# Kernel tuning notes

Measured on AMD Instinct MI355X. Metric: run time of the kernel, lower is better.

Reference implementation:

```python
import jax, jax.numpy as jnp
import numpy as np

N_NODES = 100000
N_EDGES = 640000
N_GRAPHS = 2048
HID = 128
L = 3


def setup_inputs() -> dict:
    key = jax.random.key(0)
    ks = jax.random.split(key, 24)
    f32 = jnp.float32
    x = jax.random.normal(ks[0], (N_NODES, 7), dtype=f32)
    edge_attr = jax.random.normal(ks[1], (N_EDGES, 3), dtype=f32)
    edge_index = jax.random.randint(ks[2], (2, N_EDGES), 0, N_NODES, dtype=jnp.int32)
    batch = jnp.sort(jax.random.randint(ks[3], (N_NODES,), 0, N_GRAPHS, dtype=jnp.int32))

    def lin(k, fi, fo):
        return jax.random.normal(k, (fi, fo), dtype=f32) / jnp.sqrt(jnp.asarray(fi, f32))

    inp = dict(x=x, edge_attr=edge_attr, edge_index=edge_index, batch=batch)
    inp["node_w"] = lin(ks[4], 7, HID); inp["node_b"] = jnp.zeros((HID,), f32)
    inp["ew1"] = lin(ks[5], 3, HID);   inp["eb1"] = jnp.zeros((HID,), f32)
    inp["ew2"] = lin(ks[6], HID, HID); inp["eb2"] = jnp.zeros((HID,), f32)
    inp["cw1"] = jnp.stack([lin(ks[7 + i], HID, HID) for i in range(L)])
    inp["cb1"] = jnp.zeros((L, HID), f32)
    inp["cw2"] = jnp.stack([lin(ks[10 + i], HID, HID) for i in range(L)])
    inp["cb2"] = jnp.zeros((L, HID), f32)
    inp["clw1"] = lin(ks[13], HID, 64); inp["clb1"] = jnp.zeros((64,), f32)
    inp["clw2"] = lin(ks[14], 64, 1);   inp["clb2"] = jnp.zeros((1,), f32)
    inp["rw1"] = lin(ks[15], HID, 64);  inp["rb1"] = jnp.zeros((64,), f32)
    inp["rw2"] = lin(ks[16], 64, 1);    inp["rb2"] = jnp.zeros((1,), f32)
    return inp


def reference(x, edge_attr, node_w, node_b, ew1, eb1, ew2, eb2,
              cw1, cb1, cw2, cb2, clw1, clb1, clw2, clb2,
              rw1, rb1, rw2, rb2, edge_index, batch):
    relu = jax.nn.relu
    # encoders
    h = x @ node_w + node_b                                   # [N, H]
    e = relu(edge_attr @ ew1 + eb1) @ ew2 + eb2               # [E, H]
    src, dst = edge_index[0], edge_index[1]
    for l in range(L):
        # GINEConv (eps=0): out = MLP(h_i + sum_j ReLU(h_j + e_ji))
        m = relu(h[src] + e)                                  # [E, H] gather + edge add
        agg = jax.ops.segment_sum(m, dst, num_segments=N_NODES)
        z = h + agg
        h = relu(z @ cw1[l] + cb1[l]) @ cw2[l] + cb2[l]
        h = relu(h)                                           # dropout = identity (eval)
    # global mean pool
    ones = jnp.ones((h.shape[0],), h.dtype)
    counts = jax.ops.segment_sum(ones, batch, num_segments=N_GRAPHS)
    g = jax.ops.segment_sum(h, batch, num_segments=N_GRAPHS) / jnp.maximum(counts, 1.0)[:, None]
    success_logit = (relu(g @ clw1 + clb1) @ clw2 + clb2)[:, 0]
    route_length = (relu(g @ rw1 + rb1) @ rw2 + rb2)[:, 0]
    return success_logit, route_length
```

## Files before the change

### kernel.cpp

```cpp
#include <hip/hip_runtime.h>

#define HID 128
#define LDP 136

typedef short s16x8 __attribute__((ext_vector_type(8)));
typedef float f32x4 __attribute__((ext_vector_type(4)));
typedef float f32x2 __attribute__((ext_vector_type(2)));

__device__ __forceinline__ float bf2f(unsigned int u) {
  union { unsigned int i; float f; } v; v.i = u << 16; return v.f;
}
__device__ __forceinline__ float asf(unsigned int u) {
  union { unsigned int i; float f; } v; v.i = u; return v.f;
}
__device__ __forceinline__ unsigned short f2bf(float f) {
  union { float f; unsigned int i; } v; v.f = f;
  unsigned int r = v.i + 0x7fffu + ((v.i >> 16) & 1u);
  return (unsigned short)(r >> 16);
}
__device__ __forceinline__ unsigned char f2fp8(float f) {
  unsigned int p = __builtin_amdgcn_cvt_pk_fp8_f32(f, f, 0u, false);
  return (unsigned char)(p & 0xffu);
}

__global__ void k_zero4(float4* __restrict__ p, size_t n4) {
  size_t i = (size_t)blockIdx.x * blockDim.x + threadIdx.x;
  if (i < n4) p[i] = (float4){0.f, 0.f, 0.f, 0.f};
}

__global__ void k_hist(const int* __restrict__ dst, int* __restrict__ deg, int nE) {
  int e = blockIdx.x * blockDim.x + threadIdx.x;
  if (e < nE) atomicAdd(&deg[dst[e]], 1);
}

__global__ void k_scanA(const int* __restrict__ deg, int* __restrict__ bsum) {
  __shared__ int ss[256];
  int t = threadIdx.x;
  ss[t] = deg[blockIdx.x * 256 + t];
  __syncthreads();
  for (int off = 128; off; off >>= 1) {
    if (t < off) ss[t] += ss[t + off];
    __syncthreads();
  }
  if (t == 0) bsum[blockIdx.x] = ss[0];
}

__global__ void k_scanB(const int* __restrict__ bsum, int* __restrict__ bsumx, int NB) {
  __shared__ int sd[512];
  int t = threadIdx.x;
  int v = (t < NB) ? bsum[t] : 0;
  sd[t] = v;
  __syncthreads();
  for (int off = 1; off < 512; off <<= 1) {
    int a = (t >= off) ? sd[t - off] : 0;
    __syncthreads();
    sd[t] += a;
    __syncthreads();
  }
  if (t < NB) bsumx[t] = sd[t] - v;
}

__global__ void k_scanC(const int* __restrict__ deg, const int* __restrict__ bsumx,
                        int* __restrict__ cursor, int* __restrict__ rowptr) {
  __shared__ int ss[256];
  int t = threadIdx.x, i = blockIdx.x * 256 + t;
  int v = deg[i];
  ss[t] = v;
  __syncthreads();
  for (int off = 1; off < 256; off <<= 1) {
    int a = (t >= off) ? ss[t - off] : 0;
    __syncthreads();
    ss[t] += a;
    __syncthreads();
  }
  int ex = ss[t] - v + bsumx[blockIdx.x];
  cursor[i] = ex;
  rowptr[i] = ex;
}

__global__ void k_scatter(const int* __restrict__ src, const int* __restrict__ dst,
                          int* __restrict__ cursor,
                          int* __restrict__ src_s, int* __restrict__ esort, int nE) {
  int e = blockIdx.x * blockDim.x + threadIdx.x;
  if (e >= nE) return;
  int d = dst[e];
  int pos = atomicAdd(&cursor[d], 1);
  src_s[pos] = src[e];
  esort[pos] = e;
}

__global__ void k_prep_w(const float* __restrict__ ew2, const float* __restrict__ cw1,
                         const float* __restrict__ cw2, unsigned short* __restrict__ wT) {
  int idx = blockIdx.x * blockDim.x + threadIdx.x;
  if (idx >= 7 * 16384) return;
  int m = idx >> 14, i = idx & 16383;
  int n = i >> 7, k = i & 127;
  const float* s = (m == 0) ? ew2 : (m <= 3 ? cw1 + (size_t)(m - 1) * 16384
                                            : cw2 + (size_t)(m - 4) * 16384);
  wT[idx] = f2bf(s[k * 128 + n]);
}

__global__ void k_node_enc(const float* __restrict__ x, const float* __restrict__ w,
                           const float* __restrict__ b, unsigned short* __restrict__ h16, int nN) {
  int idx = blockIdx.x * blockDim.x + threadIdx.x;
  if (idx >= nN * HID) return;
  int i = idx >> 7, j = idx & 127;
  float acc = b[j];
  const float* xr = x + (size_t)i * 7;
#pragma unroll
  for (int k = 0; k < 7; ++k) acc += xr[k] * w[k * HID + j];
  h16[idx] = f2bf(acc);
}

__global__ void __launch_bounds__(256) k_edge_gemm(
    const float* __restrict__ ea, const int* __restrict__ esort,
    const float* __restrict__ ew1, const float* __restrict__ eb1,
    const unsigned short* __restrict__ w2t, const float* __restrict__ eb2,
    unsigned char* __restrict__ e8, int nE) {
  __shared__ __attribute__((aligned(16))) unsigned short ts1[128 * LDP];
  __shared__ float eaL[384];
  __shared__ int esL[128];
  int tid = threadIdx.x;
  int e0 = blockIdx.x * 128;
  if (tid < 128) esL[tid] = esort[e0 + tid];
  __syncthreads();
  for (int i = tid; i < 384; i += 256) {
    int r = i / 3, c = i - r * 3;
    eaL[i] = ea[(size_t)esL[r] * 3 + c];
  }
  __syncthreads();
  {
    int j = tid & 127, r0 = (tid >> 7) * 64;
    float wa = ew1[j], wb = ew1[HID + j], wc = ew1[2 * HID + j], bj = eb1[j];
    for (int r = r0; r < r0 + 64; ++r) {
      float a = bj + eaL[r * 3] * wa + eaL[r * 3 + 1] * wb + eaL[r * 3 + 2] * wc;
      ts1[r * LDP + j] = f2bf(fmaxf(a, 0.f));
    }
  }
  __syncthreads();
  int wave = tid >> 6, lane = tid & 63;
  int l15 = lane & 15, quad = lane >> 4;
  int rbase = (wave >> 1) * 64, nbase = (wave & 1) * 64;
  f32x4 acc[4][4];
#pragma unroll
  for (int i = 0; i < 4; ++i)
#pragma unroll
    for (int j = 0; j < 4; ++j) acc[i][j] = (f32x4){0.f, 0.f, 0.f, 0.f};
  for (int kc = 0; kc < 4; ++kc) {
    int k0 = kc * 32 + quad * 8;
    s16x8 af[4], bf[4];
#pragma unroll
    for (int t = 0; t < 4; ++t)
      af[t] = *(const s16x8*)&ts1[(rbase + t * 16 + l15) * LDP + k0];
#pragma unroll
    for (int t = 0; t < 4; ++t)
      bf[t] = *(const s16x8*)&w2t[(size_t)(nbase + t * 16 + l15) * HID + k0];
#pragma unroll
    for (int i = 0; i < 4; ++i)
#pragma unroll
      for (int j = 0; j < 4; ++j)
        acc[i][j] = __builtin_amdgcn_mfma_f32_16x16x32_bf16(af[i], bf[j], acc[i][j], 0, 0, 0);
  }
  float ebv[4];
#pragma unroll
  for (int t = 0; t < 4; ++t) ebv[t] = eb2[nbase + t * 16 + l15];
#pragma unroll
  for (int tr = 0; tr < 4; ++tr)
#pragma unroll
    for (int reg = 0; reg < 4; ++reg) {
      int row = rbase + tr * 16 + quad * 4 + reg;
#pragma unroll
      for (int tc = 0; tc < 4; ++tc) {
        int col = nbase + tc * 16 + l15;
        e8[(size_t)(e0 + row) * HID + col] = f2fp8(acc[tr][tc][reg] + ebv[tc]);
      }
    }
}

__global__ void __launch_bounds__(256) k_conv_csr(
    const unsigned short* __restrict__ h16in, const unsigned char* __restrict__ e8,
    const int* __restrict__ src_s, const int* __restrict__ rowptr,
    const unsigned short* __restrict__ w1t, const float* __restrict__ b1,
    const unsigned short* __restrict__ w2t, const float* __restrict__ b2,
    unsigned short* __restrict__ h16out, int nN) {
  __shared__ __attribute__((aligned(16))) unsigned short zs[32 * LDP];
  __shared__ int rpS[4][12];
  int tid = threadIdx.x;
  int n0 = blockIdx.x * 32;
  int wave = tid >> 6, lane = tid & 63;
  int l15 = lane & 15, quad = lane >> 4;
  {
    int c16 = l15 * 8;
    int c2 = lane * 2;
    int wbase = wave * 8;
    int nodeBase = n0 + wbase;
    int nCnt = nN - nodeBase; if (nCnt > 8) nCnt = 8; if (nCnt < 0) nCnt = 0;
#pragma unroll
    for (int i = 0; i < 8; ++i) {
      int n = nodeBase + i;
      unsigned int hv = 0u;
      if (n < nN) hv = *(const unsigned int*)&h16in[(size_t)n * HID + c2];
      *(unsigned int*)&zs[(wbase + i) * LDP + c2] = hv;
    }
    if (lane < 9) {
      int i = (lane < nCnt) ? lane : nCnt;
      rpS[wave][lane] = (nCnt > 0) ? rowptr[nodeBase + i] : 0;
    }
    if (nCnt > 0) {
      int gb = rpS[wave][0];
      int gEnd = rpS[wave][8];
      int ni = 0;
      while (ni < 8 && rpS[wave][ni + 1] <= gb) ++ni;
      int re = (ni < 8) ? rpS[wave][ni + 1] : gb;
      float acc[8];
#pragma unroll
      for (int j = 0; j < 8; ++j) acc[j] = 0.f;

      int eixA = 0, eixB = 0, eixC = 0, svA = 0, svB = 0, svC = 0;
      int niA = 0, niB = 0, niC = 0;
      bool vA = false, vB = false, vC = false, lA = false, lB = false, lC = false;
      uint2 evA, evB;
      uint4 hvA, hvB;
      bool aA = false, aB = false, aC = false;

#define PS(eix, sv, v, l, nis)                                   \
  { int gq = gb + quad;                                          \
    eix = (gq < re) ? gq : (re - 1);                             \
    v = (gq < re);                                               \
    l = (gb + 4 >= re);                                          \
    nis = ni;                                                    \
    sv = src_s[eix];                                             \
    gb = (gb + 4 < re) ? (gb + 4) : re;                          \
    if (gb >= re) {                                              \
      while (ni < 8 && rpS[wave][ni + 1] <= gb) ++ni;            \
      if (ni < 8) re = rpS[wave][ni + 1];                        \
    } }
#define PEH(ev, hv, eix, sv)                                     \
  { ev = *(const uint2*)&e8[(size_t)eix * HID + c16];            \
    hv = *(const uint4*)&h16in[(size_t)sv * HID + c16]; }
#define FOLDX(ev, hv, v, l, nis)                                 \
  { const unsigned int* ew = (const unsigned int*)&ev;           \
    const unsigned int* hw = (const unsigned int*)&hv;           \
    if (v) {                                                     \
      _Pragma("unroll")                                          \
      for (int j = 0; j < 2; ++j) {                              \
        f32x2 pa = __builtin_amdgcn_cvt_pk_f32_fp8(ew[j], false); \
        f32x2 pb = __builtin_amdgcn_cvt_pk_f32_fp8(ew[j], true);  \
        acc[4*j+0] += fmaxf(asf(hw[2*j] << 16) + pa[0], 0.f);    \
        acc[4*j+1] += fmaxf(asf(hw[2*j] & 0xffff0000u) + pa[1], 0.f); \
        acc[4*j+2] += fmaxf(asf(hw[2*j+1] << 16) + pb[0], 0.f);  \
        acc[4*j+3] += fmaxf(asf(hw[2*j+1] & 0xffff0000u) + pb[1], 0.f); \
      }                                                          \
    }                                                            \
    if (l) {                                                     \
      _Pragma("unroll")                                          \
      for (int j = 0; j < 8; ++j) {                              \
        acc[j] += __shfl_xor(acc[j], 16);                        \
        acc[j] += __shfl_xor(acc[j], 32);                        \
      }                                                          \
      if (quad == 0) {                                           \
        int row = wbase + nis;                                   \
        uint4 z = *(const uint4*)&zs[row * LDP + c16];           \
        unsigned int* zw = (unsigned int*)&z;                    \
        _Pragma("unroll")                                        \
        for (int j = 0; j < 4; ++j) {                            \
          float z0 = asf(zw[j] << 16) + acc[2*j];                \
          float z1 = asf(zw[j] & 0xffff0000u) + acc[2*j+1];      \
          zw[j] = (unsigned int)f2bf(z0) | ((unsigned int)f2bf(z1) << 16); \
        }                                                        \
        *(uint4*)&zs[row * LDP + c16] = z;                       \
      }                                                          \
      _Pragma("unroll")                                          \
      for (int j = 0; j < 8; ++j) acc[j] = 0.f;                  \
    } }

      if (gb < gEnd) { PS(eixA, svA, vA, lA, niA) aA = true; }
      if (gb < gEnd) { PS(eixB, svB, vB, lB, niB) aB = true; }
      if (aA) PEH(evA, hvA, eixA, svA)
      while (aA) {
        aC = (gb < gEnd);
        if (aC) PS(eixC, svC, vC, lC, niC)
        if (aB) PEH(evB, hvB, eixB, svB)
        FOLDX(evA, hvA, vA, lA, niA)
        aA = aB; evA = evB; hvA = hvB; vA = vB; lA = lB; niA = niB; eixA = eixB; svA = svB;
        aB = aC; eixB = eixC; svB = svC; vB = vC; lB = lC; niB = niC;
      }
#undef PS
#undef PEH
#undef FOLDX
    }
  }
  __syncthreads();
  int rbase = (wave >> 1) * 16, nbase = (wave & 1) * 64;
  f32x4 acc[4];
#pragma unroll
  for (int j = 0; j < 4; ++j) acc[j] = (f32x4){0.f, 0.f, 0.f, 0.f};
  for (int kc = 0; kc < 4; ++kc) {
    int k0 = kc * 32 + quad * 8;
    s16x8 af, bf[4];
    af = *(const s16x8*)&zs[(rbase + l15) * LDP + k0];
#pragma unroll
    for (int t = 0; t < 4; ++t)
      bf[t] = *(const s16x8*)&w1t[(size_t)(nbase + t * 16 + l15) * HID + k0];
#pragma unroll
    for (int j = 0; j < 4; ++j)
      acc[j] = __builtin_amdgcn_mfma_f32_16x16x32_bf16(af, bf[j], acc[j], 0, 0, 0);
  }
  __syncthreads();
  {
    float bv[4];
#pragma unroll
    for (int t = 0; t < 4; ++t) bv[t] = b1[nbase + t * 16 + l15];
#pragma unroll
    for (int tc = 0; tc < 4; ++tc)
#pragma unroll
      for (int reg = 0; reg < 4; ++reg) {
        int row = rbase + quad * 4 + reg;
        int col = nbase + tc * 16 + l15;
        zs[row * LDP + col] = f2bf(fmaxf(acc[tc][reg] + bv[tc], 0.f));
      }
  }
  __syncthreads();
#pragma unroll
  for (int j = 0; j < 4; ++j) acc[j] = (f32x4){0.f, 0.f, 0.f, 0.f};
  for (int kc = 0; kc < 4; ++kc) {
    int k0 = kc * 32 + quad * 8;
    s16x8 af, bf[4];
    af = *(const s16x8*)&zs[(rbase + l15) * LDP + k0];
#pragma unroll
    for (int t = 0; t < 4; ++t)
      bf[t] = *(const s16x8*)&w2t[(size_t)(nbase + t * 16 + l15) * HID + k0];
#pragma unroll
    for (int j = 0; j < 4; ++j)
      acc[j] = __builtin_amdgcn_mfma_f32_16x16x32_bf16(af, bf[j], acc[j], 0, 0, 0);
  }
  {
    float bv[4];
#pragma unroll
    for (int t = 0; t < 4; ++t) bv[t] = b2[nbase + t * 16 + l15];
#pragma unroll
    for (int reg = 0; reg < 4; ++reg) {
      int grow = n0 + rbase + quad * 4 + reg;
      if (grow < nN) {
#pragma unroll
        for (int tc = 0; tc < 4; ++tc) {
          int col = nbase + tc * 16 + l15;
          h16out[(size_t)grow * HID + col] = f2bf(fmaxf(acc[tc][reg] + bv[tc], 0.f));
        }
      }
    }
  }
}

__global__ void k_counts(const int* __restrict__ batch, int* __restrict__ cnts, int nN) {
  int i = blockIdx.x * blockDim.x + threadIdx.x;
  if (i < nN) atomicAdd(&cnts[batch[i]], 1);
}

__global__ void __launch_bounds__(256) k_pool2(
    const unsigned short* __restrict__ h16, const int* __restrict__ batch,
    float* __restrict__ g, int nN) {
  __shared__ int bL[128];
  int tid = threadIdx.x;
  int n0 = blockIdx.x * 128;
  if (tid < 128) {
    int n = n0 + tid;
    bL[tid] = (n < nN) ? batch[n] : -1;
  }
  __syncthreads();
  int half = tid >> 7, col = tid & 127;
  int rs = half * 64;
  int cur = -1;
  float s = 0.f;
  for (int r = rs; r < rs + 64; ++r) {
    int b = bL[r];
    float v = (b >= 0) ? bf2f((unsigned int)h16[(size_t)(n0 + r) * HID + col]) : 0.f;
    if (b != cur) {
      if (cur >= 0) atomicAdd(&g[(size_t)cur * HID + col], s);
      cur = b; s = v;
    } else s += v;
  }
  if (cur >= 0) atomicAdd(&g[(size_t)cur * HID + col], s);
}

__global__ void __launch_bounds__(128) k_head(
    const float* __restrict__ g, const int* __restrict__ counts,
    const float* __restrict__ clw1, const float* __restrict__ clb1,
    const float* __restrict__ clw2, const float* __restrict__ clb2,
    const float* __restrict__ rw1, const float* __restrict__ rb1,
    const float* __restrict__ rw2, const float* __restrict__ rb2,
    float* __restrict__ out, int nG) {
  __shared__ float gs[HID];
  int b = blockIdx.x;
  int tid = threadIdx.x;
  float cnt = fmaxf((float)counts[b], 1.f);
  gs[tid] = g[b * HID + tid] / cnt;
  __syncthreads();
  int wave = tid >> 6, lane = tid & 63;
  const float* w1 = wave ? rw1 : clw1;
  const float* b1 = wave ? rb1 : clb1;
  const float* w2 = wave ? rw2 : clw2;
  const float* b2 = wave ? rb2 : clb2;
  float acc = b1[lane];
  for (int k = 0; k < HID; ++k) acc += gs[k] * w1[k * 64 + lane];
  acc = fmaxf(acc, 0.f) * w2[lane];
#pragma unroll
  for (int off = 32; off; off >>= 1) acc += __shfl_down(acc, off);
  if (lane == 0) out[wave * nG + b] = acc + b2[0];
}

extern "C" void kernel_launch(void* const* d_in, const int* in_sizes, int n_in,
                              void* d_out, int out_size, void* d_ws, size_t ws_size,
                              hipStream_t stream) {
  const float* x      = (const float*)d_in[0];
  const float* ea     = (const float*)d_in[1];
  const int*   eidx   = (const int*)d_in[2];
  const int*   batch  = (const int*)d_in[3];
  const float* node_w = (const float*)d_in[4];
  const float* node_b = (const float*)d_in[5];
  const float* ew1    = (const float*)d_in[6];
  const float* eb1    = (const float*)d_in[7];
  const float* ew2    = (const float*)d_in[8];
  const float* eb2    = (const float*)d_in[9];
  const float* cw1    = (const float*)d_in[10];
  const float* cb1    = (const float*)d_in[11];
  const float* cw2    = (const float*)d_in[12];
  const float* cb2    = (const float*)d_in[13];
  const float* clw1   = (const float*)d_in[14];
  const float* clb1   = (const float*)d_in[15];
  const float* clw2   = (const float*)d_in[16];
  const float* clb2   = (const float*)d_in[17];
  const float* rw1    = (const float*)d_in[18];
  const float* rb1    = (const float*)d_in[19];
  const float* rw2    = (const float*)d_in[20];
  const float* rb2    = (const float*)d_in[21];
  float* out = (float*)d_out;

  int nN = in_sizes[3];
  int nE = in_sizes[2] / 2;
  int nG = out_size / 2;
  const int* src = eidx;
  const int* dst = eidx + nE;

  int NB = (nN + 255) / 256;
  int bins = NB * 256;

  size_t hN = (size_t)nN * HID;
  size_t gN = (size_t)nG * HID;
  float* g    = (float*)d_ws;
  int*   cnts = (int*)(g + gN);
  unsigned short* wT   = (unsigned short*)(cnts + nG);
  unsigned short* h16a = wT + 7 * 16384;
  unsigned short* h16b = h16a + hN;
  int* deg    = (int*)(h16b + hN);
  int* cursor = deg + bins;
  int* rowptr = cursor + bins;
  int* bsum   = rowptr + bins;
  int* bsumx  = bsum + 512;
  int* src_s  = bsumx + 512;
  int* esort  = src_s + nE;
  unsigned char* e8 = (unsigned char*)(esort + nE);

  k_zero4<<<(int)((bins / 4 + 255) / 256), 256, 0, stream>>>((float4*)deg, bins / 4);
  k_hist<<<(nE + 255) / 256, 256, 0, stream>>>(dst, deg, nE);
  k_scanA<<<NB, 256, 0, stream>>>(deg, bsum);
  k_scanB<<<1, 512, 0, stream>>>(bsum, bsumx, NB);
  k_scanC<<<NB, 256, 0, stream>>>(deg, bsumx, cursor, rowptr);
  k_scatter<<<(nE + 255) / 256, 256, 0, stream>>>(src, dst, cursor, src_s, esort, nE);

  k_prep_w<<<(7 * 16384 + 255) / 256, 256, 0, stream>>>(ew2, cw1, cw2, wT);
  k_edge_gemm<<<nE / 128, 256, 0, stream>>>(ea, esort, ew1, eb1, wT, eb2, e8, nE);
  k_node_enc<<<(nN * HID + 255) / 256, 256, 0, stream>>>(x, node_w, node_b, h16a, nN);

  unsigned short* hin  = h16a;
  unsigned short* hout = h16b;
  for (int l = 0; l < 3; ++l) {
    k_conv_csr<<<(nN + 31) / 32, 256, 0, stream>>>(
        hin, e8, src_s, rowptr,
        wT + (size_t)(1 + l) * 16384, cb1 + (size_t)l * HID,
        wT + (size_t)(4 + l) * 16384, cb2 + (size_t)l * HID, hout, nN);
    unsigned short* t = hin; hin = hout; hout = t;
  }

  k_zero4<<<(int)(((gN + nG) / 4 + 255) / 256), 256, 0, stream>>>((float4*)g, (gN + nG) / 4);
  k_counts<<<(nN + 255) / 256, 256, 0, stream>>>(batch, cnts, nN);
  k_pool2<<<(nN + 127) / 128, 256, 0, stream>>>(hin, batch, g, nN);
  k_head<<<nG, 128, 0, stream>>>(g, cnts, clw1, clb1, clw2, clb2,
                                 rw1, rb1, rw2, rb2, out, nG);
}
```

Before: 595.8 us.

## Switch CSR aggregation to full-wave-per-edge with scalar rowptr and prefetch

Rewrites the gather-aggregate phase of the conv kernel so that each wave processes one edge at a time across all 64 lanes (2 columns per lane), instead of four edges in parallel across 16-lane quads with 8 columns each. Row pointers are now read into scalar registers via readfirstlane instead of shared memory, which removes the cross-quad shuffle reductions and the per-node flush logic. Source indices are prefetched four edges ahead and the edge/feature loads one edge ahead, with nontemporal loads for the edge features. The trade-off is narrower per-lane loads (4 bytes of h and 2 bytes of e) and a serial per-edge loop, which may reduce memory-level parallelism.

```diff
diff --git a/kernel.cpp b/kernel.cpp
--- a/kernel.cpp
+++ b/kernel.cpp
@@ -184,111 +184,74 @@
     const unsigned short* __restrict__ w2t, const float* __restrict__ b2,
     unsigned short* __restrict__ h16out, int nN) {
   __shared__ __attribute__((aligned(16))) unsigned short zs[32 * LDP];
-  __shared__ int rpS[4][12];
   int tid = threadIdx.x;
   int n0 = blockIdx.x * 32;
   int wave = tid >> 6, lane = tid & 63;
   int l15 = lane & 15, quad = lane >> 4;
+  int waveu = __builtin_amdgcn_readfirstlane(wave);
+  int c2 = lane * 2;
   {
-    int c16 = l15 * 8;
-    int c2 = lane * 2;
-    int wbase = wave * 8;
-    int nodeBase = n0 + wbase;
-    int nCnt = nN - nodeBase; if (nCnt > 8) nCnt = 8; if (nCnt < 0) nCnt = 0;
+    int nodeBase = n0 + waveu * 8;
 #pragma unroll
     for (int i = 0; i < 8; ++i) {
-      int n = nodeBase + i;
-      unsigned int hv = 0u;
-      if (n < nN) hv = *(const unsigned int*)&h16in[(size_t)n * HID + c2];
-      *(unsigned int*)&zs[(wbase + i) * LDP + c2] = hv;
+      int n = nodeBase + i; if (n > nN - 1) n = nN - 1;
+      unsigned int hv = *(const unsigned int*)&h16in[(size_t)n * HID + c2];
+      *(unsigned int*)&zs[(waveu * 8 + i) * LDP + c2] = hv;
     }
-    if (lane < 9) {
-      int i = (lane < nCnt) ? lane : nCnt;
-      rpS[wave][lane] = (nCnt > 0) ? rowptr[nodeBase + i] : 0;
+    int i0 = nodeBase;     if (i0 > nN) i0 = nN;
+    int i1 = nodeBase + 1; if (i1 > nN) i1 = nN;
+    int i2 = nodeBase + 2; if (i2 > nN) i2 = nN;
+    int i8 = nodeBase + 8; if (i8 > nN) i8 = nN;
+    int gb   = __builtin_amdgcn_readfirstlane(rowptr[i0]);
+    int gEnd = __builtin_amdgcn_readfirstlane(rowptr[i8]);
+    int re   = __builtin_amdgcn_readfirstlane(rowptr[i1]);
+    int reN  = __builtin_amdgcn_readfirstlane(rowptr[i2]);
+    float a0 = 0.f, a1 = 0.f;
+    int ni = 0;
+#define FLUSH_NODE(NI)                                                      \
+    { int zr = (waveu * 8 + (NI)) * LDP + c2;                               \
+      unsigned int z = *(const unsigned int*)&zs[zr];                       \
+      float z0 = asf(z << 16) + a0;                                         \
+      float z1 = asf(z & 0xffff0000u) + a1;                                 \
+      *(unsigned int*)&zs[zr] = (unsigned int)f2bf(z0) |                    \
+                                ((unsigned int)f2bf(z1) << 16);             \
+      a0 = 0.f; a1 = 0.f; }
+    if (gb < gEnd) {
+      int gL = gEnd - 1;
+      int s0 = src_s[gb];
+      int j1 = gb + 1 > gL ? gL : gb + 1;
+      int j2 = gb + 2 > gL ? gL : gb + 2;
+      int j3 = gb + 3 > gL ? gL : gb + 3;
+      int s1v = src_s[j1];
+      int s2v = src_s[j2];
+      int s3v = src_s[j3];
+      unsigned int hA = *(const unsigned int*)&h16in[(size_t)s0 * HID + c2];
+      unsigned int eA = __builtin_nontemporal_load(
+          (const unsigned short*)&e8[(size_t)gb * HID + c2]);
+      for (int e = gb; e < gEnd; ++e) {
+        int j4 = e + 4 > gL ? gL : e + 4;
+        int s4v = src_s[j4];
+        int ip = e + 1 > gL ? gL : e + 1;
+        unsigned int hB = *(const unsigned int*)&h16in[(size_t)s1v * HID + c2];
+        unsigned int eB = __builtin_nontemporal_load(
+            (const unsigned short*)&e8[(size_t)ip * HID + c2]);
+        while (ni < 8 && re <= e) {
+          FLUSH_NODE(ni)
+          ++ni;
+          re = reN;
+          int jn = nodeBase + ni + 2; if (jn > nN) jn = nN;
+          reN = __builtin_amdgcn_readfirstlane(rowptr[jn]);
+        }
+        f32x2 pe = __builtin_amdgcn_cvt_pk_f32_fp8(eA, false);
+        float h0 = asf(hA << 16);
+        float h1 = asf(hA & 0xffff0000u);
+        a0 += fmaxf(h0 + pe[0], 0.f);
+        a1 += fmaxf(h1 + pe[1], 0.f);
+        hA = hB; eA = eB; s1v = s2v; s2v = s3v; s3v = s4v;
+      }
     }
-    if (nCnt > 0) {
-      int gb = rpS[wave][0];
-      int gEnd = rpS[wave][8];
-      int ni = 0;
-      while (ni < 8 && rpS[wave][ni + 1] <= gb) ++ni;
-      int re = (ni < 8) ? rpS[wave][ni + 1] : gb;
-      float acc[8];
-#pragma unroll
-      for (int j = 0; j < 8; ++j) acc[j] = 0.f;
-
-      int eixA = 0, eixB = 0, eixC = 0, svA = 0, svB = 0, svC = 0;
-      int niA = 0, niB = 0, niC = 0;
-      bool vA = false, vB = false, vC = false, lA = false, lB = false, lC = false;
-      uint2 evA, evB;
-      uint4 hvA, hvB;
-      bool aA = false, aB = false, aC = false;
-
-#define PS(eix, sv, v, l, nis)                                   \
-  { int gq = gb + quad;                                          \
-    eix = (gq < re) ? gq : (re - 1);                             \
-    v = (gq < re);                                               \
-    l = (gb + 4 >= re);                                          \
-    nis = ni;                                                    \
-    sv = src_s[eix];                                             \
-    gb = (gb + 4 < re) ? (gb + 4) : re;                          \
-    if (gb >= re) {                                              \
-      while (ni < 8 && rpS[wave][ni + 1] <= gb) ++ni;            \
-      if (ni < 8) re = rpS[wave][ni + 1];                        \
-    } }
-#define PEH(ev, hv, eix, sv)                                     \
-  { ev = *(const uint2*)&e8[(size_t)eix * HID + c16];            \
-    hv = *(const uint4*)&h16in[(size_t)sv * HID + c16]; }
-#define FOLDX(ev, hv, v, l, nis)                                 \
-  { const unsigned int* ew = (const unsigned int*)&ev;           \
-    const unsigned int* hw = (const unsigned int*)&hv;           \
-    if (v) {                                                     \
-      _Pragma("unroll")                                          \
-      for (int j = 0; j < 2; ++j) {                              \
-        f32x2 pa = __builtin_amdgcn_cvt_pk_f32_fp8(ew[j], false); \
-        f32x2 pb = __builtin_amdgcn_cvt_pk_f32_fp8(ew[j], true);  \
-        acc[4*j+0] += fmaxf(asf(hw[2*j] << 16) + pa[0], 0.f);    \
-        acc[4*j+1] += fmaxf(asf(hw[2*j] & 0xffff0000u) + pa[1], 0.f); \
-        acc[4*j+2] += fmaxf(asf(hw[2*j+1] << 16) + pb[0], 0.f);  \
-        acc[4*j+3] += fmaxf(asf(hw[2*j+1] & 0xffff0000u) + pb[1], 0.f); \
-      }                                                          \
-    }                                                            \
-    if (l) {                                                     \
-      _Pragma("unroll")                                          \
-      for (int j = 0; j < 8; ++j) {                              \
-        acc[j] += __shfl_xor(acc[j], 16);                        \
-        acc[j] += __shfl_xor(acc[j], 32);                        \
-      }                                                          \
-      if (quad == 0) {                                           \
-        int row = wbase + nis;                                   \
-        uint4 z = *(const uint4*)&zs[row * LDP + c16];           \
-        unsigned int* zw = (unsigned int*)&z;                    \
-        _Pragma("unroll")                                        \
-        for (int j = 0; j < 4; ++j) {                            \
-          float z0 = asf(zw[j] << 16) + acc[2*j];                \
-          float z1 = asf(zw[j] & 0xffff0000u) + acc[2*j+1];      \
-          zw[j] = (unsigned int)f2bf(z0) | ((unsigned int)f2bf(z1) << 16); \
-        }                                                        \
-        *(uint4*)&zs[row * LDP + c16] = z;                       \
-      }                                                          \
-      _Pragma("unroll")                                          \
-      for (int j = 0; j < 8; ++j) acc[j] = 0.f;                  \
-    } }
-
-      if (gb < gEnd) { PS(eixA, svA, vA, lA, niA) aA = true; }
-      if (gb < gEnd) { PS(eixB, svB, vB, lB, niB) aB = true; }
-      if (aA) PEH(evA, hvA, eixA, svA)
-      while (aA) {
-        aC = (gb < gEnd);
-        if (aC) PS(eixC, svC, vC, lC, niC)
-        if (aB) PEH(evB, hvB, eixB, svB)
-        FOLDX(evA, hvA, vA, lA, niA)
-        aA = aB; evA = evB; hvA = hvB; vA = vB; lA = lB; niA = niB; eixA = eixB; svA = svB;
-        aB = aC; eixB = eixC; svB = svC; vB = vC; lB = lC; niB = niC;
-      }
-#undef PS
-#undef PEH
-#undef FOLDX
-    }
+    while (ni < 8) { FLUSH_NODE(ni) ++ni; }
+#undef FLUSH_NODE
   }
   __syncthreads();
   int rbase = (wave >> 1) * 16, nbase = (wave & 1) * 64;
```

New measurement: 712.9 us. 19.6% more time.

## Merge init kernels, single-pass atomic scan, fold counts into pooling

Applied to the files above, without the earlier changes.

Four small setup kernels (two zero fills, weight transpose/convert, node encoder) become one multi-role launch. The three-kernel scan becomes one kernel that gets each block's base offset with an atomic on a global counter. That makes rowptr non-monotone across blocks, so a per-node row-end array is added and conv reads each wave's segment end from it. Graph counts are now accumulated inside the pooling kernel, removing another launch. The aim is fewer launches and less serial scan work. The risk is that conv's edge-range logic assumes contiguous CSR ranges across the 8 nodes of a wave, which may no longer hold across 256-node block boundaries.

```diff
diff --git a/kernel.cpp b/kernel.cpp
--- a/kernel.cpp
+++ b/kernel.cpp
@@ -23,9 +23,45 @@
   return (unsigned char)(p & 0xffu);
 }
 
-__global__ void k_zero4(float4* __restrict__ p, size_t n4) {
-  size_t i = (size_t)blockIdx.x * blockDim.x + threadIdx.x;
-  if (i < n4) p[i] = (float4){0.f, 0.f, 0.f, 0.f};
+__global__ void __launch_bounds__(256) k_init(
+    float4* __restrict__ zd, int nzd4, float4* __restrict__ zg, int nzg4,
+    const float* __restrict__ ew2, const float* __restrict__ cw1,
+    const float* __restrict__ cw2, unsigned short* __restrict__ wT,
+    const float* __restrict__ x, const float* __restrict__ nw,
+    const float* __restrict__ nb, unsigned short* __restrict__ h16, int nN,
+    int bZD, int bZG, int bPW) {
+  int bid = blockIdx.x, tid = threadIdx.x;
+  if (bid < bZD) {
+    int i = bid * 256 + tid;
+    if (i < nzd4) zd[i] = (float4){0.f, 0.f, 0.f, 0.f};
+    return;
+  }
+  bid -= bZD;
+  if (bid < bZG) {
+    int i = bid * 256 + tid;
+    if (i < nzg4) zg[i] = (float4){0.f, 0.f, 0.f, 0.f};
+    return;
+  }
+  bid -= bZG;
+  if (bid < bPW) {
+    int idx = bid * 256 + tid;
+    int m = idx >> 14, i = idx & 16383;
+    int n = i >> 7, k = i & 127;
+    const float* s = (m == 0) ? ew2 : (m <= 3 ? cw1 + (size_t)(m - 1) * 16384
+                                              : cw2 + (size_t)(m - 4) * 16384);
+    wT[idx] = f2bf(s[k * 128 + n]);
+    return;
+  }
+  bid -= bPW;
+  int idx = bid * 256 + tid;
+  if (idx < nN * HID) {
+    int i = idx >> 7, j = idx & 127;
+    float acc = nb[j];
+    const float* xr = x + (size_t)i * 7;
+#pragma unroll
+    for (int k = 0; k < 7; ++k) acc += xr[k] * nw[k * HID + j];
+    h16[idx] = f2bf(acc);
+  }
 }
 
 __global__ void k_hist(const int* __restrict__ dst, int* __restrict__ deg, int nE) {
@@ -33,36 +69,11 @@
   if (e < nE) atomicAdd(&deg[dst[e]], 1);
 }
 
-__global__ void k_scanA(const int* __restrict__ deg, int* __restrict__ bsum) {
+__global__ void __launch_bounds__(256) k_scan(
+    const int* __restrict__ deg, int* __restrict__ galloc,
+    int* __restrict__ cursor, int* __restrict__ rowptr, int* __restrict__ rpe) {
   __shared__ int ss[256];
-  int t = threadIdx.x;
-  ss[t] = deg[blockIdx.x * 256 + t];
-  __syncthreads();
-  for (int off = 128; off; off >>= 1) {
-    if (t < off) ss[t] += ss[t + off];
-    __syncthreads();
-  }
-  if (t == 0) bsum[blockIdx.x] = ss[0];
-}
-
-__global__ void k_scanB(const int* __restrict__ bsum, int* __restrict__ bsumx, int NB) {
-  __shared__ int sd[512];
-  int t = threadIdx.x;
-  int v = (t < NB) ? bsum[t] : 0;
-  sd[t] = v;
-  __syncthreads();
-  for (int off = 1; off < 512; off <<= 1) {
-    int a = (t >= off) ? sd[t - off] : 0;
-    __syncthreads();
-    sd[t] += a;
-    __syncthreads();
-  }
-  if (t < NB) bsumx[t] = sd[t] - v;
-}
-
-__global__ void k_scanC(const int* __restrict__ deg, const int* __restrict__ bsumx,
-                        int* __restrict__ cursor, int* __restrict__ rowptr) {
-  __shared__ int ss[256];
+  __shared__ int sbase;
   int t = threadIdx.x, i = blockIdx.x * 256 + t;
   int v = deg[i];
   ss[t] = v;
@@ -73,9 +84,12 @@
     ss[t] += a;
     __syncthreads();
   }
-  int ex = ss[t] - v + bsumx[blockIdx.x];
+  if (t == 255) sbase = atomicAdd(galloc, ss[255]);
+  __syncthreads();
+  int ex = ss[t] - v + sbase;
   cursor[i] = ex;
   rowptr[i] = ex;
+  rpe[i] = ex + v;
 }
 
 __global__ void k_scatter(const int* __restrict__ src, const int* __restrict__ dst,
@@ -87,29 +101,6 @@
   int pos = atomicAdd(&cursor[d], 1);
   src_s[pos] = src[e];
   esort[pos] = e;
-}
-
-__global__ void k_prep_w(const float* __restrict__ ew2, const float* __restrict__ cw1,
-                         const float* __restrict__ cw2, unsigned short* __restrict__ wT) {
-  int idx = blockIdx.x * blockDim.x + threadIdx.x;
-  if (idx >= 7 * 16384) return;
-  int m = idx >> 14, i = idx & 16383;
-  int n = i >> 7, k = i & 127;
-  const float* s = (m == 0) ? ew2 : (m <= 3 ? cw1 + (size_t)(m - 1) * 16384
-                                            : cw2 + (size_t)(m - 4) * 16384);
-  wT[idx] = f2bf(s[k * 128 + n]);
-}
-
-__global__ void k_node_enc(const float* __restrict__ x, const float* __restrict__ w,
-                           const float* __restrict__ b, unsigned short* __restrict__ h16, int nN) {
-  int idx = blockIdx.x * blockDim.x + threadIdx.x;
-  if (idx >= nN * HID) return;
-  int i = idx >> 7, j = idx & 127;
-  float acc = b[j];
-  const float* xr = x + (size_t)i * 7;
-#pragma unroll
-  for (int k = 0; k < 7; ++k) acc += xr[k] * w[k * HID + j];
-  h16[idx] = f2bf(acc);
 }
 
 __global__ void __launch_bounds__(256) k_edge_gemm(
@@ -180,6 +171,7 @@
 __global__ void __launch_bounds__(256) k_conv_csr(
     const unsigned short* __restrict__ h16in, const unsigned char* __restrict__ e8,
     const int* __restrict__ src_s, const int* __restrict__ rowptr,
+    const int* __restrict__ rpe,
     const unsigned short* __restrict__ w1t, const float* __restrict__ b1,
     const unsigned short* __restrict__ w2t, const float* __restrict__ b2,
     unsigned short* __restrict__ h16out, int nN) {
@@ -202,10 +194,11 @@
       if (n < nN) hv = *(const unsigned int*)&h16in[(size_t)n * HID + c2];
       *(unsigned int*)&zs[(wbase + i) * LDP + c2] = hv;
     }
-    if (lane < 9) {
-      int i = (lane < nCnt) ? lane : nCnt;
+    if (lane < 8) {
+      int i = (lane < nCnt) ? lane : (nCnt > 0 ? nCnt - 1 : 0);
       rpS[wave][lane] = (nCnt > 0) ? rowptr[nodeBase + i] : 0;
     }
+    if (lane == 8) rpS[wave][8] = (nCnt > 0) ? rpe[nodeBase + nCnt - 1] : 0;
     if (nCnt > 0) {
       int gb = rpS[wave][0];
       int gEnd = rpS[wave][8];
@@ -352,14 +345,9 @@
   }
 }
 
-__global__ void k_counts(const int* __restrict__ batch, int* __restrict__ cnts, int nN) {
-  int i = blockIdx.x * blockDim.x + threadIdx.x;
-  if (i < nN) atomicAdd(&cnts[batch[i]], 1);
-}
-
 __global__ void __launch_bounds__(256) k_pool2(
     const unsigned short* __restrict__ h16, const int* __restrict__ batch,
-    float* __restrict__ g, int nN) {
+    float* __restrict__ g, int* __restrict__ cnts, int nN) {
   __shared__ int bL[128];
   int tid = threadIdx.x;
   int n0 = blockIdx.x * 128;
@@ -370,17 +358,23 @@
   __syncthreads();
   int half = tid >> 7, col = tid & 127;
   int rs = half * 64;
-  int cur = -1;
+  int cur = -1, rl = 0;
   float s = 0.f;
   for (int r = rs; r < rs + 64; ++r) {
     int b = bL[r];
     float v = (b >= 0) ? bf2f((unsigned int)h16[(size_t)(n0 + r) * HID + col]) : 0.f;
     if (b != cur) {
-      if (cur >= 0) atomicAdd(&g[(size_t)cur * HID + col], s);
-      cur = b; s = v;
-    } else s += v;
-  }
-  if (cur >= 0) atomicAdd(&g[(size_t)cur * HID + col], s);
+      if (cur >= 0) {
+        atomicAdd(&g[(size_t)cur * HID + col], s);
+        if (col == 0) atomicAdd(&cnts[cur], rl);
+      }
+      cur = b; s = v; rl = 1;
+    } else { s += v; ++rl; }
+  }
+  if (cur >= 0) {
+    atomicAdd(&g[(size_t)cur * HID + col], s);
+    if (col == 0) atomicAdd(&cnts[cur], rl);
+  }
 }
 
 __global__ void __launch_bounds__(128) k_head(
@@ -447,44 +441,46 @@
 
   size_t hN = (size_t)nN * HID;
   size_t gN = (size_t)nG * HID;
-  float* g    = (float*)d_ws;
-  int*   cnts = (int*)(g + gN);
-  unsigned short* wT   = (unsigned short*)(cnts + nG);
+  float* g      = (float*)d_ws;
+  int*   cnts   = (int*)(g + gN);
+  int*   galloc = cnts + nG;
+  unsigned short* wT   = (unsigned short*)(galloc + 4);
   unsigned short* h16a = wT + 7 * 16384;
   unsigned short* h16b = h16a + hN;
   int* deg    = (int*)(h16b + hN);
   int* cursor = deg + bins;
   int* rowptr = cursor + bins;
-  int* bsum   = rowptr + bins;
-  int* bsumx  = bsum + 512;
-  int* src_s  = bsumx + 512;
+  int* rpe    = rowptr + bins;
+  int* src_s  = rpe + bins;
   int* esort  = src_s + nE;
   unsigned char* e8 = (unsigned char*)(esort + nE);
 
-  k_zero4<<<(int)((bins / 4 + 255) / 256), 256, 0, stream>>>((float4*)deg, bins / 4);
+  int nzd4 = bins / 4;
+  int nzg4 = (int)((gN + nG + 4) / 4);
+  int bZD = (nzd4 + 255) / 256;
+  int bZG = (nzg4 + 255) / 256;
+  int bPW = (7 * 16384) / 256;
+  int bNE = (nN * HID + 255) / 256;
+
+  k_init<<<bZD + bZG + bPW + bNE, 256, 0, stream>>>(
+      (float4*)deg, nzd4, (float4*)g, nzg4,
+      ew2, cw1, cw2, wT, x, node_w, node_b, h16a, nN, bZD, bZG, bPW);
   k_hist<<<(nE + 255) / 256, 256, 0, stream>>>(dst, deg, nE);
-  k_scanA<<<NB, 256, 0, stream>>>(deg, bsum);
-  k_scanB<<<1, 512, 0, stream>>>(bsum, bsumx, NB);
-  k_scanC<<<NB, 256, 0, stream>>>(deg, bsumx, cursor, rowptr);
+  k_scan<<<NB, 256, 0, stream>>>(deg, galloc, cursor, rowptr, rpe);
   k_scatter<<<(nE + 255) / 256, 256, 0, stream>>>(src, dst, cursor, src_s, esort, nE);
-
-  k_prep_w<<<(7 * 16384 + 255) / 256, 256, 0, stream>>>(ew2, cw1, cw2, wT);
   k_edge_gemm<<<nE / 128, 256, 0, stream>>>(ea, esort, ew1, eb1, wT, eb2, e8, nE);
-  k_node_enc<<<(nN * HID + 255) / 256, 256, 0, stream>>>(x, node_w, node_b, h16a, nN);
 
   unsigned short* hin  = h16a;
   unsigned short* hout = h16b;
   for (int l = 0; l < 3; ++l) {
     k_conv_csr<<<(nN + 31) / 32, 256, 0, stream>>>(
-        hin, e8, src_s, rowptr,
+        hin, e8, src_s, rowptr, rpe,
         wT + (size_t)(1 + l) * 16384, cb1 + (size_t)l * HID,
         wT + (size_t)(4 + l) * 16384, cb2 + (size_t)l * HID, hout, nN);
     unsigned short* t = hin; hin = hout; hout = t;
   }
 
-  k_zero4<<<(int)(((gN + nG) / 4 + 255) / 256), 256, 0, stream>>>((float4*)g, (gN + nG) / 4);
-  k_counts<<<(nN + 255) / 256, 256, 0, stream>>>(batch, cnts, nN);
-  k_pool2<<<(nN + 127) / 128, 256, 0, stream>>>(hin, batch, g, nN);
+  k_pool2<<<(nN + 127) / 128, 256, 0, stream>>>(hin, batch, g, cnts, nN);
   k_head<<<nG, 128, 0, stream>>>(g, cnts, clw1, clb1, clw2, clb2,
                                  rw1, rb1, rw2, rb2, out, nG);
 }
```

Result: slower. 609.0 us (+2.2%).
